# Kernel tuning notes

Hardware: AMD Instinct MI355X
Metric: run time of the kernel (lower is better)

Reference implementation:

```python
import jax, jax.numpy as jnp
import numpy as np

D = 192          # d_model = d_perc = d_tech
H = 3            # n_heads
HD = D // H      # head_dim = 64
FP = 128         # fingerprint_dim
EPS_LN = 1e-5


def _layernorm(x, g, b):
    mu = jnp.mean(x, axis=-1, keepdims=True)
    var = jnp.var(x, axis=-1, keepdims=True)
    return (x - mu) * jax.lax.rsqrt(var + EPS_LN) * g + b


def setup_inputs() -> dict:
    key = jax.random.key(0)
    ks = jax.random.split(key, 32)
    B = 65536
    s = 0.05
    inp = {
        'perc_vec': jax.random.normal(ks[0], (B, D), jnp.float32),
        'tech_vec': jax.random.normal(ks[1], (B, D), jnp.float32),
        # proj_p / proj_t (torch Linear: [out, in])
        'Wp': jax.random.normal(ks[2], (D, D), jnp.float32) * s,
        'bp': jax.random.normal(ks[3], (D,), jnp.float32) * s,
        'Wt': jax.random.normal(ks[4], (D, D), jnp.float32) * s,
        'bt': jax.random.normal(ks[5], (D,), jnp.float32) * s,
        # MultiheadAttention packed in-proj [3D, D] and out-proj [D, D]
        'in_w': jax.random.normal(ks[6], (3 * D, D), jnp.float32) * s,
        'in_b': jax.random.normal(ks[7], (3 * D,), jnp.float32) * s,
        'out_w': jax.random.normal(ks[8], (D, D), jnp.float32) * s,
        'out_b': jax.random.normal(ks[9], (D,), jnp.float32) * s,
        # FFN
        'ffn_w1': jax.random.normal(ks[10], (2 * D, D), jnp.float32) * s,
        'ffn_b1': jax.random.normal(ks[11], (2 * D,), jnp.float32) * s,
        'ffn_w2': jax.random.normal(ks[12], (D, 2 * D), jnp.float32) * s,
        'ffn_b2': jax.random.normal(ks[13], (D,), jnp.float32) * s,
        # LayerNorms
        'ln1_g': jnp.ones((D,), jnp.float32),
        'ln1_b': jnp.zeros((D,), jnp.float32),
        'ln2_g': jnp.ones((D,), jnp.float32),
        'ln2_b': jnp.zeros((D,), jnp.float32),
        # classifier head
        'cls_w1': jax.random.normal(ks[14], (D, D), jnp.float32) * s,
        'cls_b1': jax.random.normal(ks[15], (D,), jnp.float32) * s,
        'cls_w2': jax.random.normal(ks[16], (3, D), jnp.float32) * s,
        'cls_b2': jax.random.normal(ks[17], (3,), jnp.float32) * s,
        # fingerprint head
        'fp_w': jax.random.normal(ks[18], (FP, D), jnp.float32) * s,
        'fp_b': jax.random.normal(ks[19], (FP,), jnp.float32) * s,
    }
    return inp


def reference(perc_vec, tech_vec, Wp, bp, Wt, bt, in_w, in_b, out_w, out_b,
              ffn_w1, ffn_b1, ffn_w2, ffn_b2, ln1_g, ln1_b, ln2_g, ln2_b,
              cls_w1, cls_b1, cls_w2, cls_b2, fp_w, fp_b):
    B = perc_vec.shape[0]
    # projections -> 2-token sequence [B, 2, D]
    p = perc_vec @ Wp.T + bp
    t = tech_vec @ Wt.T + bt
    seq = jnp.stack([p, t], axis=1)

    # self-attention (eval mode, no dropout)
    qkv = seq @ in_w.T + in_b                     # [B, 2, 3D]
    q, k, v = jnp.split(qkv, 3, axis=-1)
    q = q.reshape(B, 2, H, HD).transpose(0, 2, 1, 3)  # [B, H, 2, HD]
    k = k.reshape(B, 2, H, HD).transpose(0, 2, 1, 3)
    v = v.reshape(B, 2, H, HD).transpose(0, 2, 1, 3)
    scores = jnp.einsum('bhqd,bhkd->bhqk', q, k) / np.sqrt(HD).astype(np.float32)
    attn = jax.nn.softmax(scores, axis=-1)
    ctx = jnp.einsum('bhqk,bhkd->bhqd', attn, v)      # [B, H, 2, HD]
    ctx = ctx.transpose(0, 2, 1, 3).reshape(B, 2, D)
    attn_out = ctx @ out_w.T + out_b

    x = _layernorm(seq + attn_out, ln1_g, ln1_b)
    h = jax.nn.relu(x @ ffn_w1.T + ffn_b1)
    ffn = h @ ffn_w2.T + ffn_b2
    x = _layernorm(x + ffn, ln2_g, ln2_b)

    z = x.mean(axis=1)                                # [B, D]
    logits = jax.nn.relu(z @ cls_w1.T + cls_b1) @ cls_w2.T + cls_b2  # [B, 3]
    probs = jax.nn.sigmoid(logits)
    fp = z @ fp_w.T + fp_b
    fp = fp / jnp.maximum(jnp.linalg.norm(fp, axis=-1, keepdims=True), 1e-12)
    # (presence_p, decode_reliability, artifact_risk, fingerprint)
    return probs[:, 0:1], probs[:, 1:2], probs[:, 2:3], fp
```

## Files before the change

### kernel.cpp

```cpp
#include <hip/hip_runtime.h>
#include <hip/hip_bf16.h>
#include <math.h>

#define D 192
#define RPB 16
typedef unsigned short u16;
typedef __attribute__((ext_vector_type(8))) short short8;
typedef __attribute__((ext_vector_type(4))) float float4v;

__device__ __forceinline__ float b2f(u16 u){ union{unsigned i; float f;}c; c.i=(unsigned)u<<16; return c.f; }
__device__ __forceinline__ u16  f2b(float f){
    union{float f; unsigned i;}c; c.f=f;
    unsigned r = c.i + 0x7FFFu + ((c.i>>16)&1u);
    return (u16)(r>>16);
}

#define WP_OFF   0
#define WT_OFF   36864
#define INW_OFF  73728
#define OUTW_OFF 184320
#define FW1_OFF  221184
#define FW2_OFF  294912
#define CW1_OFF  368640
#define FPW_OFF  405504
#define W_TOTAL  430080

__global__ __launch_bounds__(256)
void cvt_weights(const float* __restrict__ Wp, const float* __restrict__ Wt,
                 const float* __restrict__ in_w, const float* __restrict__ out_w,
                 const float* __restrict__ fw1, const float* __restrict__ fw2,
                 const float* __restrict__ cw1, const float* __restrict__ fpw,
                 u16* __restrict__ ws)
{
    int idx = blockIdx.x * 256 + threadIdx.x;
    if (idx >= W_TOTAL) return;
    const float* src; int off; int K = 192;
    if      (idx < WT_OFF)   { src = Wp;   off = WP_OFF; }
    else if (idx < INW_OFF)  { src = Wt;   off = WT_OFF; }
    else if (idx < OUTW_OFF) { src = in_w; off = INW_OFF; }
    else if (idx < FW1_OFF)  { src = out_w;off = OUTW_OFF; }
    else if (idx < FW2_OFF)  { src = fw1;  off = FW1_OFF; }
    else if (idx < CW1_OFF)  { src = fw2;  off = FW2_OFF; K = 384; }
    else if (idx < FPW_OFF)  { src = cw1;  off = CW1_OFF; }
    else                     { src = fpw;  off = FPW_OFF; }
    int lin = idx - off;
    int n = lin / K, k = lin - n*K;
    int swz = ((n>>4)*(K>>5) + (k>>5))*512 + ((n&15)<<5) + (k&31);
    ws[off + swz] = f2b(src[lin]);
}

template<int KT, int MT>
__device__ __forceinline__ void load_afrags(short8 (&A)[MT][KT], const u16* base,
                                            int stride, int lane16, int quad)
{
    #pragma unroll
    for (int mt = 0; mt < MT; ++mt)
        #pragma unroll
        for (int ks = 0; ks < KT; ++ks)
            A[mt][ks] = *(const short8*)(base + (mt*16 + lane16)*stride + ks*32 + quad*8);
}

template<int KT, int MT, int NTW>
__device__ __forceinline__ void run_gemm(const short8 (&A)[MT][KT],
    const u16* __restrict__ wsb, const float* __restrict__ bias,
    u16* dst, float* dstf, int dstride,
    const u16* resid, int rstride, bool relu, int rmul, int roff,
    int wave, int lane16, int quad)
{
    #pragma unroll
    for (int i = 0; i < NTW; ++i) {
        int nt = wave + 4*i, n0 = nt*16;
        float4v c[MT];
        #pragma unroll
        for (int mt = 0; mt < MT; ++mt) c[mt] = (float4v){0.f,0.f,0.f,0.f};
        #pragma unroll
        for (int ks = 0; ks < KT; ++ks) {
            short8 b = *(const short8*)(wsb + (size_t)((nt*KT + ks)<<9) + (lane16<<5) + (quad<<3));
            #pragma unroll
            for (int mt = 0; mt < MT; ++mt)
                c[mt] = __builtin_amdgcn_mfma_f32_16x16x32_bf16(A[mt][ks], b, c[mt], 0,0,0);
        }
        float bv = bias[n0 + lane16];
        #pragma unroll
        for (int mt = 0; mt < MT; ++mt)
            #pragma unroll
            for (int ii = 0; ii < 4; ++ii) {
                int dr = (mt*16 + quad*4 + ii)*rmul + roff;
                float v = c[mt][ii] + bv;
                if (resid) v += b2f(resid[dr*rstride + n0 + lane16]);
                if (relu)  v = fmaxf(v, 0.f);
                if (dst) dst [dr*dstride + n0 + lane16] = f2b(v);
                else     dstf[dr*dstride + n0 + lane16] = v;
            }
    }
}

#define S1 200
#define SH 392
#define A_INP 0
#define A_INT 3200
#define A_SEQ 6400
#define A_Q   0
#define A_K   12800
#define A_CTX 0
#define A_X1  12800
#define A_H   0
#define A_Z   0
#define A_CH  3200
#define A_FPF 6400
#define ARENA_U16 19200

__global__ __launch_bounds__(256, 4)
void fusion_mfma_kernel(
    const float* __restrict__ perc, const float* __restrict__ tech,
    const float* __restrict__ bp,   const float* __restrict__ bt,
    const float* __restrict__ in_b, const float* __restrict__ out_b,
    const float* __restrict__ fb1,  const float* __restrict__ fb2,
    const float* __restrict__ ln1g, const float* __restrict__ ln1b,
    const float* __restrict__ ln2g, const float* __restrict__ ln2b,
    const float* __restrict__ cb1,  const float* __restrict__ cw2,
    const float* __restrict__ cb2,  const float* __restrict__ fpb,
    const u16*   __restrict__ ws,
    float* __restrict__ out, int B)
{
    __shared__ __align__(16) u16 arena[ARENA_U16];
    __shared__ float satt[16][3][4];
    __shared__ float smu[32], srs[32], srn[16];

    const int tid = threadIdx.x;
    const int wave = tid >> 6, lane = tid & 63;
    const int lane16 = lane & 15, quad = lane >> 4;
    const int row0 = blockIdx.x * RPB;
    float* fpf = (float*)(arena + A_FPF);

    #pragma unroll
    for (int it = 0; it < 3; ++it) {
        int idx = it*256 + tid;
        int arr = idx >= 384 ? 1 : 0;
        int rem = arr ? idx - 384 : idx;
        int r = rem / 24, g = rem - r*24;
        const float* src = arr ? tech : perc;
        const float4* s4 = (const float4*)(src + (size_t)(row0 + r)*D + g*8);
        float4 lo = s4[0], hi = s4[1];
        short8 o;
        o[0]=(short)f2b(lo.x); o[1]=(short)f2b(lo.y); o[2]=(short)f2b(lo.z); o[3]=(short)f2b(lo.w);
        o[4]=(short)f2b(hi.x); o[5]=(short)f2b(hi.y); o[6]=(short)f2b(hi.z); o[7]=(short)f2b(hi.w);
        *(short8*)(arena + (arr ? A_INT : A_INP) + r*S1 + g*8) = o;
    }
    __syncthreads();

    {
        short8 A1[1][6];
        load_afrags<6,1>(A1, arena + A_INP, S1, lane16, quad);
        run_gemm<6,1,3>(A1, ws + WP_OFF, bp, arena + A_SEQ, nullptr, S1,
                        nullptr, 0, false, 2, 0, wave, lane16, quad);
        load_afrags<6,1>(A1, arena + A_INT, S1, lane16, quad);
        run_gemm<6,1,3>(A1, ws + WT_OFF, bt, arena + A_SEQ, nullptr, S1,
                        nullptr, 0, false, 2, 1, wave, lane16, quad);
    }
    __syncthreads();

    float4v vreg[3][2];
    {
        short8 A2[2][6];
        load_afrags<6,2>(A2, arena + A_SEQ, S1, lane16, quad);
        run_gemm<6,2,3>(A2, ws + INW_OFF,           in_b,       arena + A_Q, nullptr, S1,
                        nullptr, 0, false, 1, 0, wave, lane16, quad);
        run_gemm<6,2,3>(A2, ws + INW_OFF + 192*192, in_b + 192, arena + A_K, nullptr, S1,
                        nullptr, 0, false, 1, 0, wave, lane16, quad);
        #pragma unroll
        for (int i = 0; i < 3; ++i) {
            int nt = wave + 4*i;
            vreg[i][0] = (float4v){0.f,0.f,0.f,0.f};
            vreg[i][1] = (float4v){0.f,0.f,0.f,0.f};
            #pragma unroll
            for (int ks = 0; ks < 6; ++ks) {
                short8 b = *(const short8*)(ws + INW_OFF + 384*192 + ((nt*6 + ks)<<9) + (lane16<<5) + (quad<<3));
                vreg[i][0] = __builtin_amdgcn_mfma_f32_16x16x32_bf16(A2[0][ks], b, vreg[i][0], 0,0,0);
                vreg[i][1] = __builtin_amdgcn_mfma_f32_16x16x32_bf16(A2[1][ks], b, vreg[i][1], 0,0,0);
            }
            float bv = in_b[384 + nt*16 + lane16];
            #pragma unroll
            for (int mt = 0; mt < 2; ++mt)
                #pragma unroll
                for (int ii = 0; ii < 4; ++ii) vreg[i][mt][ii] += bv;
        }
    }
    __syncthreads();

    if (tid < 192) {
        int r = tid / 12, rem = tid - r*12;
        int h = rem >> 2, qt = (rem >> 1) & 1, kt = rem & 1;
        const u16* qp = arena + A_Q + (2*r + qt)*S1 + h*64;
        const u16* kp = arena + A_K + (2*r + kt)*S1 + h*64;
        float s = 0.f;
        #pragma unroll
        for (int i = 0; i < 8; ++i) {
            short8 qa = *(const short8*)(qp + i*8);
            short8 ka = *(const short8*)(kp + i*8);
            #pragma unroll
            for (int j = 0; j < 8; ++j) s += b2f((u16)qa[j]) * b2f((u16)ka[j]);
        }
        s *= 0.125f;
        float so = __shfl_xor(s, 1);
        float m = fmaxf(s, so);
        float e = expf(s - m), eo = expf(so - m);
        satt[r][h][qt*2 + kt] = e / (e + eo);
    }
    __syncthreads();

    #pragma unroll
    for (int i = 0; i < 3; ++i) {
        int col = (wave + 4*i)*16 + lane16;
        int h = col >> 6;
        #pragma unroll
        for (int mt = 0; mt < 2; ++mt)
            #pragma unroll
            for (int p = 0; p < 2; ++p) {
                int R = mt*16 + quad*4 + 2*p;
                int r = R >> 1;
                float4 pa = *(const float4*)&satt[r][h][0];
                float v0 = vreg[i][mt][2*p], v1 = vreg[i][mt][2*p+1];
                arena[A_CTX + R*S1 + col]       = f2b(pa.x*v0 + pa.y*v1);
                arena[A_CTX + (R+1)*S1 + col]   = f2b(pa.z*v0 + pa.w*v1);
            }
    }
    __syncthreads();

    {
        short8 A2[2][6];
        load_afrags<6,2>(A2, arena + A_CTX, S1, lane16, quad);
        run_gemm<6,2,3>(A2, ws + OUTW_OFF, out_b, arena + A_X1, nullptr, S1,
                        arena + A_SEQ, S1, false, 1, 0, wave, lane16, quad);
    }
    __syncthreads();

    {
        int tok = tid >> 3, sub = tid & 7;
        const u16* p = arena + A_X1 + tok*S1 + sub*24;
        float s = 0.f, s2 = 0.f;
        #pragma unroll
        for (int i = 0; i < 3; ++i) {
            short8 v = *(const short8*)(p + i*8);
            #pragma unroll
            for (int j = 0; j < 8; ++j) { float y = b2f((u16)v[j]); s += y; s2 += y*y; }
        }
        s  += __shfl_xor(s, 1);  s  += __shfl_xor(s, 2);  s  += __shfl_xor(s, 4);
        s2 += __shfl_xor(s2, 1); s2 += __shfl_xor(s2, 2); s2 += __shfl_xor(s2, 4);
        if (sub == 0) {
            float mu = s * (1.f/192.f);
            float var = s2 * (1.f/192.f) - mu*mu;
            smu[tok] = mu; srs[tok] = rsqrtf(var + 1e-5f);
        }
    }
    __syncthreads();
    #pragma unroll
    for (int it = 0; it < 3; ++it) {
        int idx = it*256 + tid;
        int tok = idx / 24, g = idx - tok*24;
        float mu = smu[tok], rs = srs[tok];
        float4 ga = ((const float4*)(ln1g + g*8))[0], gb = ((const float4*)(ln1g + g*8))[1];
        float4 ba = ((const float4*)(ln1b + g*8))[0], bb = ((const float4*)(ln1b + g*8))[1];
        float gg[8]  = {ga.x,ga.y,ga.z,ga.w,gb.x,gb.y,gb.z,gb.w};
        float bbv[8] = {ba.x,ba.y,ba.z,ba.w,bb.x,bb.y,bb.z,bb.w};
        u16* p = arena + A_X1 + tok*S1 + g*8;
        short8 v = *(const short8*)p;
        short8 o;
        #pragma unroll
        for (int j = 0; j < 8; ++j)
            o[j] = (short)f2b((b2f((u16)v[j]) - mu)*rs*gg[j] + bbv[j]);
        *(short8*)p = o;
    }
    __syncthreads();

    {
        short8 A2[2][6];
        load_afrags<6,2>(A2, arena + A_X1, S1, lane16, quad);
        run_gemm<6,2,6>(A2, ws + FW1_OFF, fb1, arena + A_H, nullptr, SH,
                        nullptr, 0, true, 1, 0, wave, lane16, quad);
    }
    __syncthreads();

    {
        float4v c[3][2];
        #pragma unroll
        for (int i = 0; i < 3; ++i) { c[i][0] = (float4v){0,0,0,0}; c[i][1] = (float4v){0,0,0,0}; }
        #pragma unroll
        for (int kc = 0; kc < 2; ++kc) {
            short8 Af[2][6];
            load_afrags<6,2>(Af, arena + A_H + kc*192, SH, lane16, quad);
            #pragma unroll
            for (int i = 0; i < 3; ++i) {
                int nt = wave + 4*i;
                #pragma unroll
                for (int ks = 0; ks < 6; ++ks) {
                    short8 b = *(const short8*)(ws + FW2_OFF + ((nt*12 + kc*6 + ks)<<9) + (lane16<<5) + (quad<<3));
                    c[i][0] = __builtin_amdgcn_mfma_f32_16x16x32_bf16(Af[0][ks], b, c[i][0], 0,0,0);
                    c[i][1] = __builtin_amdgcn_mfma_f32_16x16x32_bf16(Af[1][ks], b, c[i][1], 0,0,0);
                }
            }
        }
        #pragma unroll
        for (int i = 0; i < 3; ++i) {
            int n0 = (wave + 4*i)*16;
            float bv = fb2[n0 + lane16];
            #pragma unroll
            for (int mt = 0; mt < 2; ++mt)
                #pragma unroll
                for (int ii = 0; ii < 4; ++ii) {
                    int dr = mt*16 + quad*4 + ii;
                    u16* p = arena + A_X1 + dr*S1 + n0 + lane16;
                    *p = f2b(c[i][mt][ii] + bv + b2f(*p));
                }
        }
    }
    __syncthreads();

    {
        int tok = tid >> 3, sub = tid & 7;
        const u16* p = arena + A_X1 + tok*S1 + sub*24;
        float s = 0.f, s2 = 0.f;
        #pragma unroll
        for (int i = 0; i < 3; ++i) {
            short8 v = *(const short8*)(p + i*8);
            #pragma unroll
            for (int j = 0; j < 8; ++j) { float y = b2f((u16)v[j]); s += y; s2 += y*y; }
        }
        s  += __shfl_xor(s, 1);  s  += __shfl_xor(s, 2);  s  += __shfl_xor(s, 4);
        s2 += __shfl_xor(s2, 1); s2 += __shfl_xor(s2, 2); s2 += __shfl_xor(s2, 4);
        if (sub == 0) {
            float mu = s * (1.f/192.f);
            float var = s2 * (1.f/192.f) - mu*mu;
            smu[tok] = mu; srs[tok] = rsqrtf(var + 1e-5f);
        }
    }
    __syncthreads();
    #pragma unroll
    for (int it = 0; it < 2; ++it) {
        int idx = it*256 + tid;
        if (idx < 384) {
            int r = idx / 24, g = idx - r*24;
            float mu0 = smu[2*r], rs0 = srs[2*r];
            float mu1 = smu[2*r+1], rs1 = srs[2*r+1];
            float4 ga = ((const float4*)(ln2g + g*8))[0], gb = ((const float4*)(ln2g + g*8))[1];
            float4 ba = ((const float4*)(ln2b + g*8))[0], bb = ((const float4*)(ln2b + g*8))[1];
            float gg[8]  = {ga.x,ga.y,ga.z,ga.w,gb.x,gb.y,gb.z,gb.w};
            float bbv[8] = {ba.x,ba.y,ba.z,ba.w,bb.x,bb.y,bb.z,bb.w};
            short8 x0 = *(const short8*)(arena + A_X1 + (2*r    )*S1 + g*8);
            short8 x1 = *(const short8*)(arena + A_X1 + (2*r + 1)*S1 + g*8);
            short8 o;
            #pragma unroll
            for (int j = 0; j < 8; ++j) {
                float n0 = (b2f((u16)x0[j]) - mu0)*rs0*gg[j] + bbv[j];
                float n1 = (b2f((u16)x1[j]) - mu1)*rs1*gg[j] + bbv[j];
                o[j] = (short)f2b(0.5f*(n0 + n1));
            }
            *(short8*)(arena + A_Z + r*S1 + g*8) = o;
        }
    }
    __syncthreads();

    {
        short8 A1[1][6];
        load_afrags<6,1>(A1, arena + A_Z, S1, lane16, quad);
        run_gemm<6,1,3>(A1, ws + CW1_OFF, cb1, arena + A_CH, nullptr, S1,
                        nullptr, 0, true, 1, 0, wave, lane16, quad);
        run_gemm<6,1,2>(A1, ws + FPW_OFF, fpb, nullptr, fpf, 128,
                        nullptr, 0, false, 1, 0, wave, lane16, quad);
    }
    __syncthreads();

    if (tid < 192) {
        int g4 = tid >> 2, sub = tid & 3;
        int r = g4 / 3, cc = g4 - r*3;
        const float* w = cw2 + (size_t)cc * D + sub*48;
        const u16* hr = arena + A_CH + r*S1 + sub*48;
        float a = 0.f;
        #pragma unroll
        for (int i = 0; i < 6; ++i) {
            short8 hv = *(const short8*)(hr + i*8);
            float4 w0 = ((const float4*)w)[2*i], w1 = ((const float4*)w)[2*i+1];
            float wv[8] = {w0.x,w0.y,w0.z,w0.w,w1.x,w1.y,w1.z,w1.w};
            #pragma unroll
            for (int j = 0; j < 8; ++j) a += wv[j] * b2f((u16)hv[j]);
        }
        a += __shfl_xor(a, 1); a += __shfl_xor(a, 2);
        if (sub == 0) {
            a += cb2[cc];
            out[(size_t)cc * B + (size_t)(row0 + r)] = 1.f / (1.f + expf(-a));
        }
    } else {
        int t = tid - 192;
        int r = t >> 2, sub = t & 3;
        const float4* fp4 = (const float4*)(fpf + r*128 + sub*32);
        float s2 = 0.f;
        #pragma unroll
        for (int i = 0; i < 8; ++i) {
            float4 v = fp4[i];
            s2 += v.x*v.x + v.y*v.y + v.z*v.z + v.w*v.w;
        }
        s2 += __shfl_xor(s2, 1); s2 += __shfl_xor(s2, 2);
        if (sub == 0) srn[r] = 1.f / fmaxf(sqrtf(s2), 1e-12f);
    }
    __syncthreads();

    #pragma unroll
    for (int it = 0; it < 2; ++it) {
        int idx = it*256 + tid;
        int r = idx >> 5, c = idx & 31;
        float4 v = ((const float4*)(fpf + r*128))[c];
        float sc = srn[r];
        float4 o; o.x = v.x*sc; o.y = v.y*sc; o.z = v.z*sc; o.w = v.w*sc;
        ((float4*)(out + (size_t)3*B + (size_t)(row0 + r)*128))[c] = o;
    }
}

extern "C" void kernel_launch(void* const* d_in, const int* in_sizes, int n_in,
                              void* d_out, int out_size, void* d_ws, size_t ws_size,
                              hipStream_t stream) {
    if (ws_size < (size_t)W_TOTAL * 2) return;

    const float* perc = (const float*)d_in[0];
    const float* tech = (const float*)d_in[1];
    const float* Wp   = (const float*)d_in[2];
    const float* bp   = (const float*)d_in[3];
    const float* Wt   = (const float*)d_in[4];
    const float* bt   = (const float*)d_in[5];
    const float* in_w = (const float*)d_in[6];
    const float* in_b = (const float*)d_in[7];
    const float* ow   = (const float*)d_in[8];
    const float* ob   = (const float*)d_in[9];
    const float* fw1  = (const float*)d_in[10];
    const float* fb1  = (const float*)d_in[11];
    const float* fw2  = (const float*)d_in[12];
    const float* fb2  = (const float*)d_in[13];
    const float* ln1g = (const float*)d_in[14];
    const float* ln1b = (const float*)d_in[15];
    const float* ln2g = (const float*)d_in[16];
    const float* ln2b = (const float*)d_in[17];
    const float* cw1  = (const float*)d_in[18];
    const float* cb1  = (const float*)d_in[19];
    const float* cw2  = (const float*)d_in[20];
    const float* cb2  = (const float*)d_in[21];
    const float* fpw  = (const float*)d_in[22];
    const float* fpb  = (const float*)d_in[23];

    u16* ws = (u16*)d_ws;
    int B = in_sizes[0] / D;

    hipLaunchKernelGGL(cvt_weights, dim3((W_TOTAL + 255)/256), dim3(256), 0, stream,
                       Wp, Wt, in_w, ow, fw1, fw2, cw1, fpw, ws);

    hipLaunchKernelGGL(fusion_mfma_kernel, dim3(B / RPB), dim3(256), 0, stream,
                       perc, tech, bp, bt, in_b, ob, fb1, fb2,
                       ln1g, ln1b, ln2g, ln2b, cb1, cw2, cb2, fpb,
                       ws, (float*)d_out, B);
}
```

Measured before the change: 387.1 us.

## Fuse QK scores into register epilogues and keep LayerNorm activations in registers

```diff
diff --git a/kernel.cpp b/kernel.cpp
--- a/kernel.cpp
+++ b/kernel.cpp
@@ -13,6 +13,9 @@
     union{float f; unsigned i;}c; c.f=f;
     unsigned r = c.i + 0x7FFFu + ((c.i>>16)&1u);
     return (u16)(r>>16);
+}
+__device__ __forceinline__ float sel4(float a0,float a1,float a2,float a3,int s){
+    return s==0?a0:(s==1?a1:(s==2?a2:a3));
 }
 
 #define WP_OFF   0
@@ -100,17 +103,15 @@
 #define A_INP 0
 #define A_INT 3200
 #define A_SEQ 6400
-#define A_Q   0
-#define A_K   12800
 #define A_CTX 0
-#define A_X1  12800
+#define A_X1  6400
 #define A_H   0
 #define A_Z   0
 #define A_CH  3200
 #define A_FPF 6400
-#define ARENA_U16 19200
-
-__global__ __launch_bounds__(256, 4)
+#define ARENA_U16 12800
+
+__global__ __launch_bounds__(256, 5)
 void fusion_mfma_kernel(
     const float* __restrict__ perc, const float* __restrict__ tech,
     const float* __restrict__ bp,   const float* __restrict__ bt,
@@ -124,7 +125,8 @@
     float* __restrict__ out, int B)
 {
     __shared__ __align__(16) u16 arena[ARENA_U16];
-    __shared__ float satt[16][3][4];
+    __shared__ __align__(16) float satt[16][3][4];
+    __shared__ float wavered[4][32][2];
     __shared__ float smu[32], srs[32], srn[16];
 
     const int tid = threadIdx.x;
@@ -160,131 +162,203 @@
     }
     __syncthreads();
 
-    float4v vreg[3][2];
+    short8 A2[2][6];
+    load_afrags<6,2>(A2, arena + A_SEQ, S1, lane16, quad);
     {
-        short8 A2[2][6];
-        load_afrags<6,2>(A2, arena + A_SEQ, S1, lane16, quad);
-        run_gemm<6,2,3>(A2, ws + INW_OFF,           in_b,       arena + A_Q, nullptr, S1,
-                        nullptr, 0, false, 1, 0, wave, lane16, quad);
-        run_gemm<6,2,3>(A2, ws + INW_OFF + 192*192, in_b + 192, arena + A_K, nullptr, S1,
-                        nullptr, 0, false, 1, 0, wave, lane16, quad);
+        float4v kreg[3][2];
         #pragma unroll
         for (int i = 0; i < 3; ++i) {
             int nt = wave + 4*i;
-            vreg[i][0] = (float4v){0.f,0.f,0.f,0.f};
-            vreg[i][1] = (float4v){0.f,0.f,0.f,0.f};
+            kreg[i][0] = (float4v){0,0,0,0}; kreg[i][1] = (float4v){0,0,0,0};
             #pragma unroll
             for (int ks = 0; ks < 6; ++ks) {
-                short8 b = *(const short8*)(ws + INW_OFF + 384*192 + ((nt*6 + ks)<<9) + (lane16<<5) + (quad<<3));
-                vreg[i][0] = __builtin_amdgcn_mfma_f32_16x16x32_bf16(A2[0][ks], b, vreg[i][0], 0,0,0);
-                vreg[i][1] = __builtin_amdgcn_mfma_f32_16x16x32_bf16(A2[1][ks], b, vreg[i][1], 0,0,0);
-            }
-            float bv = in_b[384 + nt*16 + lane16];
+                short8 b = *(const short8*)(ws + INW_OFF + 192*192 + ((nt*6+ks)<<9) + (lane16<<5) + (quad<<3));
+                kreg[i][0] = __builtin_amdgcn_mfma_f32_16x16x32_bf16(A2[0][ks], b, kreg[i][0], 0,0,0);
+                kreg[i][1] = __builtin_amdgcn_mfma_f32_16x16x32_bf16(A2[1][ks], b, kreg[i][1], 0,0,0);
+            }
+            float bv = in_b[192 + nt*16 + lane16];
             #pragma unroll
             for (int mt = 0; mt < 2; ++mt)
                 #pragma unroll
-                for (int ii = 0; ii < 4; ++ii) vreg[i][mt][ii] += bv;
-        }
-    }
-    __syncthreads();
-
-    if (tid < 192) {
-        int r = tid / 12, rem = tid - r*12;
-        int h = rem >> 2, qt = (rem >> 1) & 1, kt = rem & 1;
-        const u16* qp = arena + A_Q + (2*r + qt)*S1 + h*64;
-        const u16* kp = arena + A_K + (2*r + kt)*S1 + h*64;
-        float s = 0.f;
-        #pragma unroll
-        for (int i = 0; i < 8; ++i) {
-            short8 qa = *(const short8*)(qp + i*8);
-            short8 ka = *(const short8*)(kp + i*8);
-            #pragma unroll
-            for (int j = 0; j < 8; ++j) s += b2f((u16)qa[j]) * b2f((u16)ka[j]);
-        }
-        s *= 0.125f;
-        float so = __shfl_xor(s, 1);
-        float m = fmaxf(s, so);
-        float e = expf(s - m), eo = expf(so - m);
-        satt[r][h][qt*2 + kt] = e / (e + eo);
+                for (int ii = 0; ii < 4; ++ii) kreg[i][mt][ii] += bv;
+        }
+        float* satt_w = (float*)arena;
+        #pragma unroll
+        for (int i = 0; i < 3; ++i) {
+            int nt = wave + 4*i;
+            float4v cq[2] = {(float4v){0,0,0,0},(float4v){0,0,0,0}};
+            #pragma unroll
+            for (int ks = 0; ks < 6; ++ks) {
+                short8 b = *(const short8*)(ws + INW_OFF + ((nt*6+ks)<<9) + (lane16<<5) + (quad<<3));
+                cq[0] = __builtin_amdgcn_mfma_f32_16x16x32_bf16(A2[0][ks], b, cq[0], 0,0,0);
+                cq[1] = __builtin_amdgcn_mfma_f32_16x16x32_bf16(A2[1][ks], b, cq[1], 0,0,0);
+            }
+            float bv = in_b[nt*16 + lane16];
+            float sc[2][2][4];
+            #pragma unroll
+            for (int mt = 0; mt < 2; ++mt)
+                #pragma unroll
+                for (int p = 0; p < 2; ++p) {
+                    float q0 = cq[mt][2*p] + bv, q1 = cq[mt][2*p+1] + bv;
+                    float k0 = kreg[i][mt][2*p], k1 = kreg[i][mt][2*p+1];
+                    sc[mt][p][0] = q0*k0; sc[mt][p][1] = q0*k1;
+                    sc[mt][p][2] = q1*k0; sc[mt][p][3] = q1*k1;
+                }
+            #pragma unroll
+            for (int mt = 0; mt < 2; ++mt)
+                #pragma unroll
+                for (int p = 0; p < 2; ++p)
+                    #pragma unroll
+                    for (int c = 0; c < 4; ++c) {
+                        float v = sc[mt][p][c];
+                        v += __shfl_xor(v, 1); v += __shfl_xor(v, 2);
+                        v += __shfl_xor(v, 4); v += __shfl_xor(v, 8);
+                        sc[mt][p][c] = v;
+                    }
+            if ((lane16 >> 2) == i) {
+                int c = lane16 & 3;
+                #pragma unroll
+                for (int mt = 0; mt < 2; ++mt)
+                    #pragma unroll
+                    for (int p = 0; p < 2; ++p) {
+                        float vv = sel4(sc[mt][p][0], sc[mt][p][1], sc[mt][p][2], sc[mt][p][3], c);
+                        satt_w[(wave*16 + (2*quad + p + 8*mt))*12 + i*4 + c] = vv;
+                    }
+            }
+        }
+    }
+    __syncthreads();
+
+    if (tid < 96) {
+        const float* satt_w = (const float*)arena;
+        int r = tid / 6, rem = tid - r*6;
+        int h = rem >> 1, qt = rem & 1;
+        float s0 = 0.f, s1 = 0.f;
+        #pragma unroll
+        for (int w = 0; w < 4; ++w) {
+            s0 += satt_w[(w*16 + r)*12 + h*4 + qt*2 + 0];
+            s1 += satt_w[(w*16 + r)*12 + h*4 + qt*2 + 1];
+        }
+        s0 *= 0.125f; s1 *= 0.125f;
+        float m = fmaxf(s0, s1);
+        float e0 = expf(s0 - m), e1 = expf(s1 - m);
+        float inv = 1.f / (e0 + e1);
+        satt[r][h][qt*2 + 0] = e0 * inv;
+        satt[r][h][qt*2 + 1] = e1 * inv;
+    }
+    __syncthreads();
+
+    #pragma unroll
+    for (int i = 0; i < 3; ++i) {
+        int nt = wave + 4*i, col = nt*16 + lane16;
+        float4v cv[2] = {(float4v){0,0,0,0},(float4v){0,0,0,0}};
+        #pragma unroll
+        for (int ks = 0; ks < 6; ++ks) {
+            short8 b = *(const short8*)(ws + INW_OFF + 384*192 + ((nt*6+ks)<<9) + (lane16<<5) + (quad<<3));
+            cv[0] = __builtin_amdgcn_mfma_f32_16x16x32_bf16(A2[0][ks], b, cv[0], 0,0,0);
+            cv[1] = __builtin_amdgcn_mfma_f32_16x16x32_bf16(A2[1][ks], b, cv[1], 0,0,0);
+        }
+        float bv = in_b[384 + col];
+        #pragma unroll
+        for (int mt = 0; mt < 2; ++mt)
+            #pragma unroll
+            for (int p = 0; p < 2; ++p) {
+                float v0 = cv[mt][2*p] + bv, v1 = cv[mt][2*p+1] + bv;
+                int r = 2*quad + p + 8*mt;
+                float4 pa = *(const float4*)&satt[r][i][0];
+                arena[A_CTX + (2*r    )*S1 + col] = f2b(pa.x*v0 + pa.y*v1);
+                arena[A_CTX + (2*r + 1)*S1 + col] = f2b(pa.z*v0 + pa.w*v1);
+            }
+    }
+    __syncthreads();
+
+    float4v x1r[3][2];
+    {
+        short8 Ac[2][6];
+        load_afrags<6,2>(Ac, arena + A_CTX, S1, lane16, quad);
+        #pragma unroll
+        for (int i = 0; i < 3; ++i) {
+            int nt = wave + 4*i, col = nt*16 + lane16;
+            x1r[i][0] = (float4v){0,0,0,0}; x1r[i][1] = (float4v){0,0,0,0};
+            #pragma unroll
+            for (int ks = 0; ks < 6; ++ks) {
+                short8 b = *(const short8*)(ws + OUTW_OFF + ((nt*6+ks)<<9) + (lane16<<5) + (quad<<3));
+                x1r[i][0] = __builtin_amdgcn_mfma_f32_16x16x32_bf16(Ac[0][ks], b, x1r[i][0], 0,0,0);
+                x1r[i][1] = __builtin_amdgcn_mfma_f32_16x16x32_bf16(Ac[1][ks], b, x1r[i][1], 0,0,0);
+            }
+            float bv = out_b[col];
+            #pragma unroll
+            for (int mt = 0; mt < 2; ++mt)
+                #pragma unroll
+                for (int ii = 0; ii < 4; ++ii) {
+                    int row = quad*4 + ii + 16*mt;
+                    x1r[i][mt][ii] += bv + b2f(arena[A_SEQ + row*S1 + col]);
+                }
+        }
+        float sr[2][4], s2r[2][4];
+        #pragma unroll
+        for (int mt = 0; mt < 2; ++mt)
+            #pragma unroll
+            for (int ii = 0; ii < 4; ++ii) {
+                float a0 = x1r[0][mt][ii], a1 = x1r[1][mt][ii], a2 = x1r[2][mt][ii];
+                float s = a0 + a1 + a2;
+                float s2 = a0*a0 + a1*a1 + a2*a2;
+                s  += __shfl_xor(s, 1);  s  += __shfl_xor(s, 2);
+                s  += __shfl_xor(s, 4);  s  += __shfl_xor(s, 8);
+                s2 += __shfl_xor(s2, 1); s2 += __shfl_xor(s2, 2);
+                s2 += __shfl_xor(s2, 4); s2 += __shfl_xor(s2, 8);
+                sr[mt][ii] = s; s2r[mt][ii] = s2;
+            }
+        int l = lane16;
+        float rowlo = sel4(sr[0][0], sr[0][1], sr[0][2], sr[0][3], l & 3);
+        float rowhi = sel4(sr[1][0], sr[1][1], sr[1][2], sr[1][3], l & 3);
+        float row2lo = sel4(s2r[0][0], s2r[0][1], s2r[0][2], s2r[0][3], l & 3);
+        float row2hi = sel4(s2r[1][0], s2r[1][1], s2r[1][2], s2r[1][3], l & 3);
+        float sv = (l & 4) ? rowhi : rowlo;
+        float s2v = (l & 4) ? row2hi : row2lo;
+        float val = (l & 8) ? s2v : sv;
+        wavered[wave][quad*4 + (l & 3) + 16*((l >> 2) & 1)][l >> 3] = val;
+    }
+    __syncthreads();
+    if (tid < 32) {
+        float s = 0.f, s2 = 0.f;
+        #pragma unroll
+        for (int w = 0; w < 4; ++w) { s += wavered[w][tid][0]; s2 += wavered[w][tid][1]; }
+        float mu = s * (1.f/192.f);
+        float var = s2 * (1.f/192.f) - mu*mu;
+        smu[tid] = mu; srs[tid] = rsqrtf(var + 1e-5f);
     }
     __syncthreads();
 
     #pragma unroll
     for (int i = 0; i < 3; ++i) {
         int col = (wave + 4*i)*16 + lane16;
-        int h = col >> 6;
+        float g = ln1g[col], bb = ln1b[col];
         #pragma unroll
         for (int mt = 0; mt < 2; ++mt)
             #pragma unroll
-            for (int p = 0; p < 2; ++p) {
-                int R = mt*16 + quad*4 + 2*p;
-                int r = R >> 1;
-                float4 pa = *(const float4*)&satt[r][h][0];
-                float v0 = vreg[i][mt][2*p], v1 = vreg[i][mt][2*p+1];
-                arena[A_CTX + R*S1 + col]       = f2b(pa.x*v0 + pa.y*v1);
-                arena[A_CTX + (R+1)*S1 + col]   = f2b(pa.z*v0 + pa.w*v1);
+            for (int ii = 0; ii < 4; ++ii) {
+                int row = quad*4 + ii + 16*mt;
+                float x = (x1r[i][mt][ii] - smu[row]) * srs[row] * g + bb;
+                x1r[i][mt][ii] = x;
+                arena[A_X1 + row*S1 + col] = f2b(x);
             }
     }
     __syncthreads();
 
     {
-        short8 A2[2][6];
-        load_afrags<6,2>(A2, arena + A_CTX, S1, lane16, quad);
-        run_gemm<6,2,3>(A2, ws + OUTW_OFF, out_b, arena + A_X1, nullptr, S1,
-                        arena + A_SEQ, S1, false, 1, 0, wave, lane16, quad);
+        short8 Ax[2][6];
+        load_afrags<6,2>(Ax, arena + A_X1, S1, lane16, quad);
+        __syncthreads();
+        run_gemm<6,2,6>(Ax, ws + FW1_OFF, fb1, arena + A_H, nullptr, SH,
+                        nullptr, 0, true, 1, 0, wave, lane16, quad);
     }
     __syncthreads();
 
     {
-        int tok = tid >> 3, sub = tid & 7;
-        const u16* p = arena + A_X1 + tok*S1 + sub*24;
-        float s = 0.f, s2 = 0.f;
-        #pragma unroll
-        for (int i = 0; i < 3; ++i) {
-            short8 v = *(const short8*)(p + i*8);
-            #pragma unroll
-            for (int j = 0; j < 8; ++j) { float y = b2f((u16)v[j]); s += y; s2 += y*y; }
-        }
-        s  += __shfl_xor(s, 1);  s  += __shfl_xor(s, 2);  s  += __shfl_xor(s, 4);
-        s2 += __shfl_xor(s2, 1); s2 += __shfl_xor(s2, 2); s2 += __shfl_xor(s2, 4);
-        if (sub == 0) {
-            float mu = s * (1.f/192.f);
-            float var = s2 * (1.f/192.f) - mu*mu;
-            smu[tok] = mu; srs[tok] = rsqrtf(var + 1e-5f);
-        }
-    }
-    __syncthreads();
-    #pragma unroll
-    for (int it = 0; it < 3; ++it) {
-        int idx = it*256 + tid;
-        int tok = idx / 24, g = idx - tok*24;
-        float mu = smu[tok], rs = srs[tok];
-        float4 ga = ((const float4*)(ln1g + g*8))[0], gb = ((const float4*)(ln1g + g*8))[1];
-        float4 ba = ((const float4*)(ln1b + g*8))[0], bb = ((const float4*)(ln1b + g*8))[1];
-        float gg[8]  = {ga.x,ga.y,ga.z,ga.w,gb.x,gb.y,gb.z,gb.w};
-        float bbv[8] = {ba.x,ba.y,ba.z,ba.w,bb.x,bb.y,bb.z,bb.w};
-        u16* p = arena + A_X1 + tok*S1 + g*8;
-        short8 v = *(const short8*)p;
-        short8 o;
-        #pragma unroll
-        for (int j = 0; j < 8; ++j)
-            o[j] = (short)f2b((b2f((u16)v[j]) - mu)*rs*gg[j] + bbv[j]);
-        *(short8*)p = o;
-    }
-    __syncthreads();
-
-    {
-        short8 A2[2][6];
-        load_afrags<6,2>(A2, arena + A_X1, S1, lane16, quad);
-        run_gemm<6,2,6>(A2, ws + FW1_OFF, fb1, arena + A_H, nullptr, SH,
-                        nullptr, 0, true, 1, 0, wave, lane16, quad);
-    }
-    __syncthreads();
-
-    {
-        float4v c[3][2];
-        #pragma unroll
-        for (int i = 0; i < 3; ++i) { c[i][0] = (float4v){0,0,0,0}; c[i][1] = (float4v){0,0,0,0}; }
+        float4v c2[3][2];
+        #pragma unroll
+        for (int i = 0; i < 3; ++i) { c2[i][0] = (float4v){0,0,0,0}; c2[i][1] = (float4v){0,0,0,0}; }
         #pragma unroll
         for (int kc = 0; kc < 2; ++kc) {
             short8 Af[2][6];
@@ -295,67 +369,66 @@
                 #pragma unroll
                 for (int ks = 0; ks < 6; ++ks) {
                     short8 b = *(const short8*)(ws + FW2_OFF + ((nt*12 + kc*6 + ks)<<9) + (lane16<<5) + (quad<<3));
-                    c[i][0] = __builtin_amdgcn_mfma_f32_16x16x32_bf16(Af[0][ks], b, c[i][0], 0,0,0);
-                    c[i][1] = __builtin_amdgcn_mfma_f32_16x16x32_bf16(Af[1][ks], b, c[i][1], 0,0,0);
+                    c2[i][0] = __builtin_amdgcn_mfma_f32_16x16x32_bf16(Af[0][ks], b, c2[i][0], 0,0,0);
+                    c2[i][1] = __builtin_amdgcn_mfma_f32_16x16x32_bf16(Af[1][ks], b, c2[i][1], 0,0,0);
                 }
             }
         }
         #pragma unroll
         for (int i = 0; i < 3; ++i) {
-            int n0 = (wave + 4*i)*16;
-            float bv = fb2[n0 + lane16];
+            float bv = fb2[(wave + 4*i)*16 + lane16];
             #pragma unroll
             for (int mt = 0; mt < 2; ++mt)
                 #pragma unroll
-                for (int ii = 0; ii < 4; ++ii) {
-                    int dr = mt*16 + quad*4 + ii;
-                    u16* p = arena + A_X1 + dr*S1 + n0 + lane16;
-                    *p = f2b(c[i][mt][ii] + bv + b2f(*p));
-                }
-        }
-    }
-    __syncthreads();
-
-    {
-        int tok = tid >> 3, sub = tid & 7;
-        const u16* p = arena + A_X1 + tok*S1 + sub*24;
-        float s = 0.f, s2 = 0.f;
-        #pragma unroll
-        for (int i = 0; i < 3; ++i) {
-            short8 v = *(const short8*)(p + i*8);
-            #pragma unroll
-            for (int j = 0; j < 8; ++j) { float y = b2f((u16)v[j]); s += y; s2 += y*y; }
-        }
-        s  += __shfl_xor(s, 1);  s  += __shfl_xor(s, 2);  s  += __shfl_xor(s, 4);
-        s2 += __shfl_xor(s2, 1); s2 += __shfl_xor(s2, 2); s2 += __shfl_xor(s2, 4);
-        if (sub == 0) {
+                for (int ii = 0; ii < 4; ++ii)
+                    c2[i][mt][ii] += bv + x1r[i][mt][ii];
+        }
+        float sr[2][4], s2r[2][4];
+        #pragma unroll
+        for (int mt = 0; mt < 2; ++mt)
+            #pragma unroll
+            for (int ii = 0; ii < 4; ++ii) {
+                float a0 = c2[0][mt][ii], a1 = c2[1][mt][ii], a2 = c2[2][mt][ii];
+                float s = a0 + a1 + a2;
+                float s2 = a0*a0 + a1*a1 + a2*a2;
+                s  += __shfl_xor(s, 1);  s  += __shfl_xor(s, 2);
+                s  += __shfl_xor(s, 4);  s  += __shfl_xor(s, 8);
+                s2 += __shfl_xor(s2, 1); s2 += __shfl_xor(s2, 2);
+                s2 += __shfl_xor(s2, 4); s2 += __shfl_xor(s2, 8);
+                sr[mt][ii] = s; s2r[mt][ii] = s2;
+            }
+        int l = lane16;
+        float rowlo = sel4(sr[0][0], sr[0][1], sr[0][2], sr[0][3], l & 3);
+        float rowhi = sel4(sr[1][0], sr[1][1], sr[1][2], sr[1][3], l & 3);
+        float row2lo = sel4(s2r[0][0], s2r[0][1], s2r[0][2], s2r[0][3], l & 3);
+        float row2hi = sel4(s2r[1][0], s2r[1][1], s2r[1][2], s2r[1][3], l & 3);
+        float sv = (l & 4) ? rowhi : rowlo;
+        float s2v = (l & 4) ? row2hi : row2lo;
+        float val = (l & 8) ? s2v : sv;
+        wavered[wave][quad*4 + (l & 3) + 16*((l >> 2) & 1)][l >> 3] = val;
+        __syncthreads();
+        if (tid < 32) {
+            float s = 0.f, s2 = 0.f;
+            #pragma unroll
+            for (int w = 0; w < 4; ++w) { s += wavered[w][tid][0]; s2 += wavered[w][tid][1]; }
             float mu = s * (1.f/192.f);
             float var = s2 * (1.f/192.f) - mu*mu;
-            smu[tok] = mu; srs[tok] = rsqrtf(var + 1e-5f);
-        }
-    }
-    __syncthreads();
-    #pragma unroll
-    for (int it = 0; it < 2; ++it) {
-        int idx = it*256 + tid;
-        if (idx < 384) {
-            int r = idx / 24, g = idx - r*24;
-            float mu0 = smu[2*r], rs0 = srs[2*r];
-            float mu1 = smu[2*r+1], rs1 = srs[2*r+1];
-            float4 ga = ((const float4*)(ln2g + g*8))[0], gb = ((const float4*)(ln2g + g*8))[1];
-            float4 ba = ((const float4*)(ln2b + g*8))[0], bb = ((const float4*)(ln2b + g*8))[1];
-            float gg[8]  = {ga.x,ga.y,ga.z,ga.w,gb.x,gb.y,gb.z,gb.w};
-            float bbv[8] = {ba.x,ba.y,ba.z,ba.w,bb.x,bb.y,bb.z,bb.w};
-            short8 x0 = *(const short8*)(arena + A_X1 + (2*r    )*S1 + g*8);
-            short8 x1 = *(const short8*)(arena + A_X1 + (2*r + 1)*S1 + g*8);
-            short8 o;
-            #pragma unroll
-            for (int j = 0; j < 8; ++j) {
-                float n0 = (b2f((u16)x0[j]) - mu0)*rs0*gg[j] + bbv[j];
-                float n1 = (b2f((u16)x1[j]) - mu1)*rs1*gg[j] + bbv[j];
-                o[j] = (short)f2b(0.5f*(n0 + n1));
-            }
-            *(short8*)(arena + A_Z + r*S1 + g*8) = o;
+            smu[tid] = mu; srs[tid] = rsqrtf(var + 1e-5f);
+        }
+        __syncthreads();
+        #pragma unroll
+        for (int i = 0; i < 3; ++i) {
+            int col = (wave + 4*i)*16 + lane16;
+            float g = ln2g[col], bb = ln2b[col];
+            #pragma unroll
+            for (int mt = 0; mt < 2; ++mt)
+                #pragma unroll
+                for (int p = 0; p < 2; ++p) {
+                    int r = 2*quad + p + 8*mt;
+                    float n0v = (c2[i][mt][2*p]   - smu[2*r  ]) * srs[2*r  ] * g + bb;
+                    float n1v = (c2[i][mt][2*p+1] - smu[2*r+1]) * srs[2*r+1] * g + bb;
+                    arena[A_Z + r*S1 + col] = f2b(0.5f*(n0v + n1v));
+                }
         }
     }
     __syncthreads();
```

Result: slower. 516.8 us (+33.5%).
